# Kernel tuning notes

Measured on AMD Instinct MI355X. Metric: run time of the kernel, lower is better.

## Reference

```python
import jax, jax.numpy as jnp
import numpy as np

N_CONS = 100000
N_VARS = 200000
N_EDGES = 2000000
EMB = 64


def _emb(x, w0, b0, w1, b1):
    # Linear -> ReLU -> Linear -> ReLU
    h = jnp.maximum(x @ w0 + b0, 0.0)
    return jnp.maximum(h @ w1 + b1, 0.0)


def _bgc(left, src, dst, ef, right, lw, lb, ew, rw, fw, fb, ow0, ob0, ow1, ob1):
    # message: final(ReLU)(left_lin(right[dst]) + edge_lin(ef) + right_lin(left[src]))
    pre = right[dst] @ lw + lb + ef @ ew + left[src] @ rw          # [E, EMB]
    msg = jnp.maximum(pre, 0.0) @ fw + fb                          # [E, EMB]
    agg = jax.ops.segment_sum(msg, dst, num_segments=right.shape[0])  # [n_right, EMB]
    h = jnp.concatenate([agg, right], axis=-1)                     # [n_right, 2*EMB]
    return jnp.maximum(h @ ow0 + ob0, 0.0) @ ow1 + ob1


def setup_inputs() -> dict:
    key = jax.random.key(0)
    kit = iter(jax.random.split(key, 64))
    f32 = jnp.float32
    def W(i, o):
        return (jax.random.normal(next(kit), (i, o), f32) / np.float32(np.sqrt(i))).astype(f32)
    def B(o):
        return jnp.zeros((o,), f32)

    d = {}
    d['constraint_features'] = jax.random.normal(next(kit), (N_CONS, 5), f32)
    ei_c = jax.random.randint(next(kit), (N_EDGES,), 0, N_CONS)
    ei_v = jax.random.randint(next(kit), (N_EDGES,), 0, N_VARS)
    d['edge_indices'] = jnp.stack([ei_c, ei_v]).astype(jnp.int32)  # [2, E]
    d['edge_features'] = jax.random.normal(next(kit), (N_EDGES, 1), f32)
    d['variable_features'] = jax.random.normal(next(kit), (N_VARS, 19), f32)

    # cons / var embeddings
    d['cw0'], d['cb0'], d['cw1'], d['cb1'] = W(5, EMB), B(EMB), W(EMB, EMB), B(EMB)
    d['vw0'], d['vb0'], d['vw1'], d['vb1'] = W(19, EMB), B(EMB), W(EMB, EMB), B(EMB)
    # two bipartite convs
    for p in ('vc', 'cv'):
        d[p + '_lw'], d[p + '_lb'] = W(EMB, EMB), B(EMB)
        d[p + '_ew'] = W(1, EMB)
        d[p + '_rw'] = W(EMB, EMB)
        d[p + '_fw'], d[p + '_fb'] = W(EMB, EMB), B(EMB)
        d[p + '_ow0'], d[p + '_ob0'] = W(2 * EMB, EMB), B(EMB)
        d[p + '_ow1'], d[p + '_ob1'] = W(EMB, EMB), B(EMB)
    # policy head (final Linear has no bias)
    d['pw0'], d['pb0'], d['pw1'] = W(EMB, EMB), B(EMB), W(EMB, 1)
    # value head
    d['vhw0'], d['vhb0'], d['vhw1'], d['vhb1'] = W(EMB, EMB), B(EMB), W(EMB, 1), B(1)
    return d


def reference(constraint_features, edge_indices, edge_features, variable_features,
              cw0, cb0, cw1, cb1, vw0, vb0, vw1, vb1,
              vc_lw, vc_lb, vc_ew, vc_rw, vc_fw, vc_fb, vc_ow0, vc_ob0, vc_ow1, vc_ob1,
              cv_lw, cv_lb, cv_ew, cv_rw, cv_fw, cv_fb, cv_ow0, cv_ob0, cv_ow1, cv_ob1,
              pw0, pb0, pw1, vhw0, vhb0, vhw1, vhb1):
    cons_idx = edge_indices[0]
    var_idx = edge_indices[1]
    c = _emb(constraint_features, cw0, cb0, cw1, cb1)  # [n_cons, EMB]
    v = _emb(variable_features, vw0, vb0, vw1, vb1)    # [n_vars, EMB]
    # v -> c (reversed edges: src=var, dst=cons)
    c = _bgc(v, var_idx, cons_idx, edge_features, c,
             vc_lw, vc_lb, vc_ew, vc_rw, vc_fw, vc_fb, vc_ow0, vc_ob0, vc_ow1, vc_ob1)
    # c -> v (src=cons, dst=var)
    v = _bgc(c, cons_idx, var_idx, edge_features, v,
             cv_lw, cv_lb, cv_ew, cv_rw, cv_fw, cv_fb, cv_ow0, cv_ob0, cv_ow1, cv_ob1)
    policy = (jnp.maximum(v @ pw0 + pb0, 0.0) @ pw1).squeeze(-1)   # [n_vars]
    value = (jnp.maximum(v @ vhw0 + vhb0, 0.0) @ vhw1 + vhb1).squeeze(-1)  # [n_vars]
    return (value, policy)
```

## Files before the change

kernel.cpp:

```cpp
#include <hip/hip_runtime.h>

typedef unsigned short u16;

#define RN  128
#define RSH 7
#define CAP 6400
#define NBINS_MAX 4096

__device__ __forceinline__ float bf2f(u16 u) {
    return __uint_as_float(((unsigned int)u) << 16);
}
__device__ __forceinline__ u16 f2bf(float f) {
    unsigned int x = __float_as_uint(f);
    return (u16)((x + 0x7fffu + ((x >> 16) & 1u)) >> 16);
}

__device__ __forceinline__ void mm64(const float* A, const float* B, float* C, int lane)
{
    float bcol[64];
#pragma unroll
    for (int m = 0; m < 64; ++m) bcol[m] = B[m*64 + lane];
    for (int k = 0; k < 64; ++k) {
        float acc = 0.f;
#pragma unroll
        for (int m = 0; m < 64; ++m) acc = fmaf(A[k*64 + m], bcol[m], acc);
        C[k*64 + lane] = acc;
    }
}

__device__ __forceinline__ void vm64(const float* a, const float* B, const float* add,
                                     float* c, int lane)
{
    float acc = (add != 0) ? add[lane] : 0.f;
#pragma unroll
    for (int m = 0; m < 64; ++m) acc = fmaf(a[m], B[m*64 + lane], acc);
    c[lane] = acc;
}

__global__ __launch_bounds__(256) void prep_kernel(
    const float* vc_fw, const float* vc_fb, const float* vc_ow0,
    const float* vc_ow1, const float* vc_ob1,
    const float* cv_rw, const float* cv_fw, const float* cv_fb,
    const float* cv_ow0, const float* cv_ow1, const float* cv_ob1,
    const float* pw0, const float* pb0, const float* vhw0, const float* vhb0,
    float* Fc, float* gc, float* Hc, float* hc, float* Fv, float* gv,
    float* Pw, float* pbp, float* Vw, float* vbp)
{
    const int wv = threadIdx.x >> 6;
    const int lane = threadIdx.x & 63;
    if (wv == 0) {
        mm64(vc_fw, vc_ow0, Fc, lane);
        vm64(vc_fb, vc_ow0, 0, gc, lane);
    } else if (wv == 1) {
        mm64(vc_ow1, cv_rw, Hc, lane);
        vm64(vc_ob1, cv_rw, 0, hc, lane);
    } else if (wv == 2) {
        mm64(cv_fw, cv_ow0, Fv, lane);
        vm64(cv_fb, cv_ow0, 0, gv, lane);
    } else {
        mm64(cv_ow1, pw0, Pw, lane);
        vm64(cv_ob1, pw0, pb0, pbp, lane);
        mm64(cv_ow1, vhw0, Vw, lane);
        vm64(cv_ob1, vhw0, vhb0, vbp, lane);
    }
}

__global__ __launch_bounds__(256) void embc_kernel(
    const float* __restrict__ X,
    const float* __restrict__ W0, const float* __restrict__ B0,
    const float* __restrict__ W1, const float* __restrict__ B1,
    const float* __restrict__ LW, const float* __restrict__ LB,
    u16* __restrict__ c0out, float* __restrict__ RlOut, int M)
{
    const int lane = threadIdx.x & 63;
    const int wv   = threadIdx.x >> 6;
    __shared__ __align__(16) float xs[4][8*5];
    __shared__ __align__(16) float hb[4][8][64];
    __shared__ __align__(16) float yb[4][8][64];
    const int rowTile = (blockIdx.x*4 + wv)*8;

    for (int idx = lane; idx < 8*5; idx += 64) {
        long gi = (long)rowTile*5 + idx;
        xs[wv][idx] = (gi < (long)M*5) ? X[gi] : 0.f;
    }
    {
        float w0[5];
#pragma unroll
        for (int k = 0; k < 5; ++k) w0[k] = W0[k*64 + lane];
        const float b0 = B0[lane];
#pragma unroll
        for (int r = 0; r < 8; ++r) {
            float acc = b0;
#pragma unroll
            for (int k = 0; k < 5; ++k) acc = fmaf(xs[wv][r*5 + k], w0[k], acc);
            hb[wv][r][lane] = fmaxf(acc, 0.f);
        }
    }
    {
        float w1[64];
#pragma unroll
        for (int k = 0; k < 64; ++k) w1[k] = W1[k*64 + lane];
        const float b1 = B1[lane];
#pragma unroll
        for (int r = 0; r < 8; ++r) {
            float acc = b1;
#pragma unroll
            for (int k4 = 0; k4 < 16; ++k4) {
                float4 h4 = *(const float4*)&hb[wv][r][k4*4];
                acc = fmaf(h4.x, w1[k4*4+0], acc);
                acc = fmaf(h4.y, w1[k4*4+1], acc);
                acc = fmaf(h4.z, w1[k4*4+2], acc);
                acc = fmaf(h4.w, w1[k4*4+3], acc);
            }
            float y = fmaxf(acc, 0.f);
            yb[wv][r][lane] = y;
            int row = rowTile + r;
            if (row < M) c0out[(size_t)row*64 + lane] = f2bf(y);
        }
    }
    {
        float w[64];
#pragma unroll
        for (int k = 0; k < 64; ++k) w[k] = LW[k*64 + lane];
        const float bb = LB[lane];
#pragma unroll
        for (int r = 0; r < 8; ++r) {
            float acc = bb;
#pragma unroll
            for (int k4 = 0; k4 < 16; ++k4) {
                float4 y4 = *(const float4*)&yb[wv][r][k4*4];
                acc = fmaf(y4.x, w[k4*4+0], acc);
                acc = fmaf(y4.y, w[k4*4+1], acc);
                acc = fmaf(y4.z, w[k4*4+2], acc);
                acc = fmaf(y4.w, w[k4*4+3], acc);
            }
            int row = rowTile + r;
            if (row < M) RlOut[(size_t)row*64 + lane] = acc;
        }
    }
}

__global__ __launch_bounds__(256) void embv_kernel(
    const float* __restrict__ X,
    const float* __restrict__ W0, const float* __restrict__ B0,
    const float* __restrict__ W1, const float* __restrict__ B1,
    const float* __restrict__ RW,
    const float* __restrict__ LW, const float* __restrict__ LB,
    u16* __restrict__ v0out, u16* __restrict__ LsOut,
    float* __restrict__ RlOut, int M)
{
    const int lane = threadIdx.x & 63;
    const int wv   = threadIdx.x >> 6;
    __shared__ __align__(16) float xs[4][8*19];
    __shared__ __align__(16) float hb[4][8][64];
    __shared__ __align__(16) float yb[4][8][64];
    const int rowTile = (blockIdx.x*4 + wv)*8;

    for (int idx = lane; idx < 8*19; idx += 64) {
        long gi = (long)rowTile*19 + idx;
        xs[wv][idx] = (gi < (long)M*19) ? X[gi] : 0.f;
    }
    {
        float w0[19];
#pragma unroll
        for (int k = 0; k < 19; ++k) w0[k] = W0[k*64 + lane];
        const float b0 = B0[lane];
#pragma unroll
        for (int r = 0; r < 8; ++r) {
            float acc = b0;
#pragma unroll
            for (int k = 0; k < 19; ++k) acc = fmaf(xs[wv][r*19 + k], w0[k], acc);
            hb[wv][r][lane] = fmaxf(acc, 0.f);
        }
    }
    {
        float w1[64];
#pragma unroll
        for (int k = 0; k < 64; ++k) w1[k] = W1[k*64 + lane];
        const float b1 = B1[lane];
#pragma unroll
        for (int r = 0; r < 8; ++r) {
            float acc = b1;
#pragma unroll
            for (int k4 = 0; k4 < 16; ++k4) {
                float4 h4 = *(const float4*)&hb[wv][r][k4*4];
                acc = fmaf(h4.x, w1[k4*4+0], acc);
                acc = fmaf(h4.y, w1[k4*4+1], acc);
                acc = fmaf(h4.z, w1[k4*4+2], acc);
                acc = fmaf(h4.w, w1[k4*4+3], acc);
            }
            float y = fmaxf(acc, 0.f);
            yb[wv][r][lane] = y;
            int row = rowTile + r;
            if (row < M) v0out[(size_t)row*64 + lane] = f2bf(y);
        }
    }
    {
        float w[64];
#pragma unroll
        for (int k = 0; k < 64; ++k) w[k] = RW[k*64 + lane];
#pragma unroll
        for (int r = 0; r < 8; ++r) {
            float acc = 0.f;
#pragma unroll
            for (int k4 = 0; k4 < 16; ++k4) {
                float4 y4 = *(const float4*)&yb[wv][r][k4*4];
                acc = fmaf(y4.x, w[k4*4+0], acc);
                acc = fmaf(y4.y, w[k4*4+1], acc);
                acc = fmaf(y4.z, w[k4*4+2], acc);
                acc = fmaf(y4.w, w[k4*4+3], acc);
            }
            int row = rowTile + r;
            if (row < M) LsOut[(size_t)row*64 + lane] = f2bf(acc);
        }
    }
    {
        float w[64];
#pragma unroll
        for (int k = 0; k < 64; ++k) w[k] = LW[k*64 + lane];
        const float bb = LB[lane];
#pragma unroll
        for (int r = 0; r < 8; ++r) {
            float acc = bb;
#pragma unroll
            for (int k4 = 0; k4 < 16; ++k4) {
                float4 y4 = *(const float4*)&yb[wv][r][k4*4];
                acc = fmaf(y4.x, w[k4*4+0], acc);
                acc = fmaf(y4.y, w[k4*4+1], acc);
                acc = fmaf(y4.z, w[k4*4+2], acc);
                acc = fmaf(y4.w, w[k4*4+3], acc);
            }
            int row = rowTile + r;
            if (row < M) RlOut[(size_t)row*64 + lane] = acc;
        }
    }
}

__global__ __launch_bounds__(256) void hist2_kernel(
    const int* __restrict__ eic, const int* __restrict__ eiv,
    int* cntC, int* cntV, int E)
{
    int e = blockIdx.x*256 + threadIdx.x;
    if (e >= E) return;
    atomicAdd(&cntC[eic[e]], 1);
    atomicAdd(&cntV[eiv[e]], 1);
}

__global__ __launch_bounds__(256) void coarse_kernel(
    const int* __restrict__ cnt, int N, int nb, int* cOff, int* cur)
{
    __shared__ int cs[2049];
    for (int i = threadIdx.x; i < nb; i += 256) {
        int s = 0;
        int basei = i << RSH;
        int lim = N - basei; if (lim > RN) lim = RN;
        for (int j = 0; j < lim; ++j) s += cnt[basei + j];
        cs[i] = s;
    }
    __syncthreads();
    if (threadIdx.x == 0) {
        int a = 0;
        for (int i = 0; i < nb; ++i) { int t = cs[i]; cs[i] = a; a += t; }
        cs[nb] = a;
    }
    __syncthreads();
    for (int i = threadIdx.x; i < nb; i += 256) { cOff[i] = cs[i]; cur[i] = cs[i]; }
    if (threadIdx.x == 0) cOff[nb] = cs[nb];
}

__global__ __launch_bounds__(256) void binscatter_kernel(
    const int* __restrict__ eic, const int* __restrict__ eiv,
    const float* __restrict__ ef,
    int* curC, int* curV,
    uint2* __restrict__ bC, uint2* __restrict__ bV,
    int nbC, int nbV, int E)
{
    __shared__ int bins[NBINS_MAX];
    const int nb = nbC + nbV;
    const int chunk = (E + (int)gridDim.x - 1) / (int)gridDim.x;
    const int e0 = blockIdx.x * chunk;
    int e1 = e0 + chunk; if (e1 > E) e1 = E;

    for (int i = threadIdx.x; i < nb; i += 256) bins[i] = 0;
    __syncthreads();

    for (int e = e0 + threadIdx.x; e < e1; e += 256) {
        atomicAdd(&bins[eic[e] >> RSH], 1);
        atomicAdd(&bins[nbC + (eiv[e] >> RSH)], 1);
    }
    __syncthreads();

    for (int i = threadIdx.x; i < nbC; i += 256) {
        int c = bins[i];
        bins[i] = (c > 0) ? atomicAdd(&curC[i], c) : 0;
    }
    for (int i = threadIdx.x; i < nbV; i += 256) {
        int c = bins[nbC + i];
        bins[nbC + i] = (c > 0) ? atomicAdd(&curV[i], c) : 0;
    }
    __syncthreads();

    for (int e = e0 + threadIdx.x; e < e1; e += 256) {
        const int c = eic[e], v = eiv[e];
        const unsigned fb = __float_as_uint(ef[e]) & 0xFFFFFF80u;
        int pc = atomicAdd(&bins[c >> RSH], 1);
        bC[pc] = make_uint2((unsigned)v, fb | (unsigned)(c & (RN - 1)));
        int pv = atomicAdd(&bins[nbC + (v >> RSH)], 1);
        bV[pv] = make_uint2((unsigned)c, fb | (unsigned)(v & (RN - 1)));
    }
}

__global__ __launch_bounds__(256) void aggsort_kernel(
    const int* __restrict__ cOff, const uint2* __restrict__ bucket,
    float* RlA, const u16* __restrict__ Lsb,
    const float* __restrict__ ew, int N)
{
    const int b = blockIdx.x;
    const int lane = threadIdx.x & 63;
    const int wv   = threadIdx.x >> 6;
    const int n0 = b << RSH;
    int nn = N - n0; if (nn > RN) nn = RN;

    __shared__ uint2 recS[CAP];
    __shared__ int cntS[RN];
    __shared__ int offS[RN + 1];

    const int e0 = cOff[b];
    int ec = cOff[b + 1] - e0;
    if (ec > CAP) ec = CAP;

    for (int i = threadIdx.x; i < RN; i += 256) cntS[i] = 0;
    __syncthreads();
    for (int i = threadIdx.x; i < ec; i += 256) {
        uint2 q = bucket[e0 + i];
        atomicAdd(&cntS[q.y & (RN - 1)], 1);
    }
    __syncthreads();
    if (threadIdx.x == 0) {
        int a = 0;
        for (int i = 0; i < RN; ++i) { offS[i] = a; a += cntS[i]; }
        offS[RN] = a;
    }
    __syncthreads();
    for (int i = threadIdx.x; i < RN; i += 256) cntS[i] = offS[i];
    __syncthreads();
    for (int i = threadIdx.x; i < ec; i += 256) {
        uint2 q = bucket[e0 + i];
        int p = atomicAdd(&cntS[q.y & (RN - 1)], 1);
        recS[p] = q;
    }
    __syncthreads();

    const float w = ew[lane];
    for (int r = wv; r < nn; r += 4) {
        const int s0 = offS[r], s1 = offS[r + 1];
        const float rl = RlA[(size_t)(n0 + r)*64 + lane];
        float acc = 0.f;
        int j = s0;
        for (; j + 8 <= s1; j += 8) {
            uint2 q0 = recS[j+0], q1 = recS[j+1], q2 = recS[j+2], q3 = recS[j+3];
            uint2 q4 = recS[j+4], q5 = recS[j+5], q6 = recS[j+6], q7 = recS[j+7];
            float l0 = bf2f(Lsb[(size_t)q0.x*64 + lane]);
            float l1 = bf2f(Lsb[(size_t)q1.x*64 + lane]);
            float l2 = bf2f(Lsb[(size_t)q2.x*64 + lane]);
            float l3 = bf2f(Lsb[(size_t)q3.x*64 + lane]);
            float l4 = bf2f(Lsb[(size_t)q4.x*64 + lane]);
            float l5 = bf2f(Lsb[(size_t)q5.x*64 + lane]);
            float l6 = bf2f(Lsb[(size_t)q6.x*64 + lane]);
            float l7 = bf2f(Lsb[(size_t)q7.x*64 + lane]);
            float f0 = __uint_as_float(q0.y & 0xFFFFFF80u);
            float f1 = __uint_as_float(q1.y & 0xFFFFFF80u);
            float f2 = __uint_as_float(q2.y & 0xFFFFFF80u);
            float f3 = __uint_as_float(q3.y & 0xFFFFFF80u);
            float f4 = __uint_as_float(q4.y & 0xFFFFFF80u);
            float f5 = __uint_as_float(q5.y & 0xFFFFFF80u);
            float f6 = __uint_as_float(q6.y & 0xFFFFFF80u);
            float f7 = __uint_as_float(q7.y & 0xFFFFFF80u);
            acc += fmaxf(fmaf(f0, w, rl + l0), 0.f);
            acc += fmaxf(fmaf(f1, w, rl + l1), 0.f);
            acc += fmaxf(fmaf(f2, w, rl + l2), 0.f);
            acc += fmaxf(fmaf(f3, w, rl + l3), 0.f);
            acc += fmaxf(fmaf(f4, w, rl + l4), 0.f);
            acc += fmaxf(fmaf(f5, w, rl + l5), 0.f);
            acc += fmaxf(fmaf(f6, w, rl + l6), 0.f);
            acc += fmaxf(fmaf(f7, w, rl + l7), 0.f);
        }
        for (; j < s1; ++j) {
            uint2 q = recS[j];
            float l = bf2f(Lsb[(size_t)q.x*64 + lane]);
            float f = __uint_as_float(q.y & 0xFFFFFF80u);
            acc += fmaxf(fmaf(f, w, rl + l), 0.f);
        }
        RlA[(size_t)(n0 + r)*64 + lane] = acc;
    }
}

__global__ __launch_bounds__(256, 1) void consupd_kernel(
    const float* __restrict__ aggpre, const u16* __restrict__ c0,
    const int* __restrict__ deg,
    const float* __restrict__ Fc, const float* __restrict__ OW0B,
    const float* __restrict__ gc, const float* __restrict__ ob0,
    const float* __restrict__ Hc, const float* __restrict__ hc,
    u16* __restrict__ LsOut, int M)
{
    const int lane = threadIdx.x & 63;
    const int wv   = threadIdx.x >> 6;
    __shared__ __align__(16) float xs[4][8][64];
    __shared__ __align__(16) float cs[4][8][64];
    const int rowTile = (blockIdx.x*4 + wv)*8;

    float degv[8];
#pragma unroll
    for (int r = 0; r < 8; ++r) {
        int row = rowTile + r;
        int grow = (row < M) ? row : (M - 1);
        xs[wv][r][lane] = aggpre[(size_t)grow*64 + lane];
        cs[wv][r][lane] = bf2f(c0[(size_t)grow*64 + lane]);
        degv[r] = (float)deg[grow];
    }
    {
        float wa[64], wb[64];
#pragma unroll
        for (int k = 0; k < 64; ++k) { wa[k] = Fc[k*64 + lane]; wb[k] = OW0B[k*64 + lane]; }
        const float g_l = gc[lane], b_l = ob0[lane];
#pragma unroll
        for (int r = 0; r < 8; ++r) {
            float acc = fmaf(degv[r], g_l, b_l);
#pragma unroll
            for (int k4 = 0; k4 < 16; ++k4) {
                float4 x4 = *(const float4*)&xs[wv][r][k4*4];
                float4 c4 = *(const float4*)&cs[wv][r][k4*4];
                acc = fmaf(x4.x, wa[k4*4+0], acc); acc = fmaf(c4.x, wb[k4*4+0], acc);
                acc = fmaf(x4.y, wa[k4*4+1], acc); acc = fmaf(c4.y, wb[k4*4+1], acc);
                acc = fmaf(x4.z, wa[k4*4+2], acc); acc = fmaf(c4.z, wb[k4*4+2], acc);
                acc = fmaf(x4.w, wa[k4*4+3], acc); acc = fmaf(c4.w, wb[k4*4+3], acc);
            }
            xs[wv][r][lane] = fmaxf(acc, 0.f);
        }
    }
    {
        float wh[64];
#pragma unroll
        for (int k = 0; k < 64; ++k) wh[k] = Hc[k*64 + lane];
        const float h_l = hc[lane];
#pragma unroll
        for (int r = 0; r < 8; ++r) {
            float acc = h_l;
#pragma unroll
            for (int k4 = 0; k4 < 16; ++k4) {
                float4 u4 = *(const float4*)&xs[wv][r][k4*4];
                acc = fmaf(u4.x, wh[k4*4+0], acc);
                acc = fmaf(u4.y, wh[k4*4+1], acc);
                acc = fmaf(u4.z, wh[k4*4+2], acc);
                acc = fmaf(u4.w, wh[k4*4+3], acc);
            }
            int row = rowTile + r;
            if (row < M) LsOut[(size_t)row*64 + lane] = f2bf(acc);
        }
    }
}

__global__ __launch_bounds__(256, 1) void varupdhead_kernel(
    const float* __restrict__ aggpre, const u16* __restrict__ v0,
    const int* __restrict__ deg,
    const float* __restrict__ Fv, const float* __restrict__ OW0B,
    const float* __restrict__ gv, const float* __restrict__ ob0,
    const float* __restrict__ Pw, const float* __restrict__ pbp, const float* __restrict__ pw1,
    const float* __restrict__ Vw, const float* __restrict__ vbp, const float* __restrict__ vw1,
    const float* __restrict__ vb1,
    float* __restrict__ out, int M)
{
    const int lane = threadIdx.x & 63;
    const int wv   = threadIdx.x >> 6;
    __shared__ __align__(16) float xs[4][8][64];
    __shared__ __align__(16) float cs[4][8][64];
    const int rowTile = (blockIdx.x*4 + wv)*8;

    float degv[8];
#pragma unroll
    for (int r = 0; r < 8; ++r) {
        int row = rowTile + r;
        int grow = (row < M) ? row : (M - 1);
        xs[wv][r][lane] = aggpre[(size_t)grow*64 + lane];
        cs[wv][r][lane] = bf2f(v0[(size_t)grow*64 + lane]);
        degv[r] = (float)deg[grow];
    }
    {
        float wa[64], wb[64];
#pragma unroll
        for (int k = 0; k < 64; ++k) { wa[k] = Fv[k*64 + lane]; wb[k] = OW0B[k*64 + lane]; }
        const float g_l = gv[lane], b_l = ob0[lane];
#pragma unroll
        for (int r = 0; r < 8; ++r) {
            float acc = fmaf(degv[r], g_l, b_l);
#pragma unroll
            for (int k4 = 0; k4 < 16; ++k4) {
                float4 x4 = *(const float4*)&xs[wv][r][k4*4];
                float4 c4 = *(const float4*)&cs[wv][r][k4*4];
                acc = fmaf(x4.x, wa[k4*4+0], acc); acc = fmaf(c4.x, wb[k4*4+0], acc);
                acc = fmaf(x4.y, wa[k4*4+1], acc); acc = fmaf(c4.y, wb[k4*4+1], acc);
                acc = fmaf(x4.z, wa[k4*4+2], acc); acc = fmaf(c4.z, wb[k4*4+2], acc);
                acc = fmaf(x4.w, wa[k4*4+3], acc); acc = fmaf(c4.w, wb[k4*4+3], acc);
            }
            xs[wv][r][lane] = fmaxf(acc, 0.f);
        }
    }
    {
        float wp[64], wq[64];
#pragma unroll
        for (int k = 0; k < 64; ++k) { wp[k] = Pw[k*64 + lane]; wq[k] = Vw[k*64 + lane]; }
        const float pb_l = pbp[lane], vb_l = vbp[lane];
        const float p1w = pw1[lane], v1w = vw1[lane];
        const float vbias = vb1[0];
#pragma unroll
        for (int r = 0; r < 8; ++r) {
            float tp = pb_l, tv = vb_l;
#pragma unroll
            for (int k4 = 0; k4 < 16; ++k4) {
                float4 u4 = *(const float4*)&xs[wv][r][k4*4];
                tp = fmaf(u4.x, wp[k4*4+0], tp); tv = fmaf(u4.x, wq[k4*4+0], tv);
                tp = fmaf(u4.y, wp[k4*4+1], tp); tv = fmaf(u4.y, wq[k4*4+1], tv);
                tp = fmaf(u4.z, wp[k4*4+2], tp); tv = fmaf(u4.z, wq[k4*4+2], tv);
                tp = fmaf(u4.w, wp[k4*4+3], tp); tv = fmaf(u4.w, wq[k4*4+3], tv);
            }
            tp = fmaxf(tp, 0.f) * p1w;
            tv = fmaxf(tv, 0.f) * v1w;
#pragma unroll
            for (int m = 32; m >= 1; m >>= 1) {
                tp += __shfl_xor(tp, m, 64);
                tv += __shfl_xor(tv, m, 64);
            }
            int row = rowTile + r;
            if (lane == 0 && row < M) {
                out[row]     = tv + vbias;
                out[M + row] = tp;
            }
        }
    }
}

#define AL256(x) (((x) + 255) & ~(size_t)255)

extern "C" void kernel_launch(void* const* d_in, const int* in_sizes, int n_in,
                              void* d_out, int out_size, void* d_ws, size_t ws_size,
                              hipStream_t stream)
{
    const float* cf  = (const float*)d_in[0];
    const int*   ei  = (const int*)  d_in[1];
    const float* ef  = (const float*)d_in[2];
    const float* vf  = (const float*)d_in[3];

    const float* cw0 = (const float*)d_in[4];
    const float* cb0 = (const float*)d_in[5];
    const float* cw1 = (const float*)d_in[6];
    const float* cb1 = (const float*)d_in[7];
    const float* vw0 = (const float*)d_in[8];
    const float* vb0 = (const float*)d_in[9];
    const float* vw1 = (const float*)d_in[10];
    const float* vb1 = (const float*)d_in[11];

    const float* vc_lw  = (const float*)d_in[12];
    const float* vc_lb  = (const float*)d_in[13];
    const float* vc_ew  = (const float*)d_in[14];
    const float* vc_rw  = (const float*)d_in[15];
    const float* vc_fw  = (const float*)d_in[16];
    const float* vc_fb  = (const float*)d_in[17];
    const float* vc_ow0 = (const float*)d_in[18];
    const float* vc_ob0 = (const float*)d_in[19];
    const float* vc_ow1 = (const float*)d_in[20];
    const float* vc_ob1 = (const float*)d_in[21];

    const float* cv_lw  = (const float*)d_in[22];
    const float* cv_lb  = (const float*)d_in[23];
    const float* cv_ew  = (const float*)d_in[24];
    const float* cv_rw  = (const float*)d_in[25];
    const float* cv_fw  = (const float*)d_in[26];
    const float* cv_fb  = (const float*)d_in[27];
    const float* cv_ow0 = (const float*)d_in[28];
    const float* cv_ob0 = (const float*)d_in[29];
    const float* cv_ow1 = (const float*)d_in[30];
    const float* cv_ob1 = (const float*)d_in[31];

    const float* pw0  = (const float*)d_in[32];
    const float* pb0  = (const float*)d_in[33];
    const float* pw1  = (const float*)d_in[34];
    const float* vhw0 = (const float*)d_in[35];
    const float* vhb0 = (const float*)d_in[36];
    const float* vhw1 = (const float*)d_in[37];
    const float* vhb1 = (const float*)d_in[38];

    const int NC = in_sizes[0] / 5;
    const int E  = in_sizes[1] / 2;
    const int NV = in_sizes[3] / 19;
    const int* eic = ei;
    const int* eiv = ei + E;

    const int nbC = (NC + RN - 1) >> RSH;
    const int nbV = (NV + RN - 1) >> RSH;

    char* base = (char*)d_ws;
    size_t o = 0;
    float*  RlC = (float*)(base + o);  o += AL256((size_t)NC*64*4);
    u16*    c0b = (u16*)  (base + o);  o += AL256((size_t)NC*64*2);
    u16*    LsC = (u16*)  (base + o);  o += AL256((size_t)NC*64*2);
    float*  RlV = (float*)(base + o);  o += AL256((size_t)NV*64*4);
    u16*    v0b = (u16*)  (base + o);  o += AL256((size_t)NV*64*2);
    u16*    LsV = (u16*)  (base + o);  o += AL256((size_t)NV*64*2);
    uint2*  bktC = (uint2*)(base + o); o += AL256((size_t)E*8);
    uint2*  bktV = (uint2*)(base + o); o += AL256((size_t)E*8);
    int* cntC  = (int*)(base + o);  o += AL256((size_t)NC*4);
    int* cntV  = (int*)(base + o);  o += AL256((size_t)NV*4);
    int* cOffC = (int*)(base + o);  o += AL256(((size_t)nbC + 1)*4);
    int* curC  = (int*)(base + o);  o += AL256((size_t)nbC*4);
    int* cOffV = (int*)(base + o);  o += AL256(((size_t)nbV + 1)*4);
    int* curV  = (int*)(base + o);  o += AL256((size_t)nbV*4);
    float* Fc  = (float*)(base + o); o += AL256((size_t)4096*4);
    float* Hc  = (float*)(base + o); o += AL256((size_t)4096*4);
    float* Fv  = (float*)(base + o); o += AL256((size_t)4096*4);
    float* Pw  = (float*)(base + o); o += AL256((size_t)4096*4);
    float* Vw  = (float*)(base + o); o += AL256((size_t)4096*4);
    float* gc  = (float*)(base + o); o += AL256((size_t)64*4);
    float* hc  = (float*)(base + o); o += AL256((size_t)64*4);
    float* gv  = (float*)(base + o); o += AL256((size_t)64*4);
    float* pbp = (float*)(base + o); o += AL256((size_t)64*4);
    float* vbp = (float*)(base + o); o += AL256((size_t)64*4);

    if (o > ws_size) return;
    if (nbC + nbV > NBINS_MAX) return;

    dim3 blk(256);
    dim3 gRowsC((unsigned)((NC + 31) / 32));
    dim3 gRowsV((unsigned)((NV + 31) / 32));
    dim3 gE((unsigned)((E + 255) / 256));

    (void)hipMemsetAsync(cntC, 0, (size_t)NC*4, stream);
    (void)hipMemsetAsync(cntV, 0, (size_t)NV*4, stream);
    hist2_kernel<<<gE, blk, 0, stream>>>(eic, eiv, cntC, cntV, E);
    coarse_kernel<<<dim3(1), blk, 0, stream>>>(cntC, NC, nbC, cOffC, curC);
    coarse_kernel<<<dim3(1), blk, 0, stream>>>(cntV, NV, nbV, cOffV, curV);

    prep_kernel<<<dim3(1), blk, 0, stream>>>(
        vc_fw, vc_fb, vc_ow0, vc_ow1, vc_ob1,
        cv_rw, cv_fw, cv_fb, cv_ow0, cv_ow1, cv_ob1,
        pw0, pb0, vhw0, vhb0,
        Fc, gc, Hc, hc, Fv, gv, Pw, pbp, Vw, vbp);

    embc_kernel<<<gRowsC, blk, 0, stream>>>(cf, cw0, cb0, cw1, cb1,
                                            vc_lw, vc_lb, c0b, RlC, NC);
    embv_kernel<<<gRowsV, blk, 0, stream>>>(vf, vw0, vb0, vw1, vb1,
                                            vc_rw, cv_lw, cv_lb, v0b, LsV, RlV, NV);

    binscatter_kernel<<<dim3(128), blk, 0, stream>>>(eic, eiv, ef, curC, curV,
                                                     bktC, bktV, nbC, nbV, E);

    aggsort_kernel<<<dim3((unsigned)nbC), blk, 0, stream>>>(cOffC, bktC, RlC, LsV, vc_ew, NC);
    consupd_kernel<<<gRowsC, blk, 0, stream>>>(RlC, c0b, cntC,
                                               Fc, vc_ow0 + 64*64, gc, vc_ob0,
                                               Hc, hc, LsC, NC);

    aggsort_kernel<<<dim3((unsigned)nbV), blk, 0, stream>>>(cOffV, bktV, RlV, LsC, cv_ew, NV);
    varupdhead_kernel<<<gRowsV, blk, 0, stream>>>(RlV, v0b, cntV,
                                                  Fv, cv_ow0 + 64*64, gv, cv_ob0,
                                                  Pw, pbp, pw1, Vw, vbp, vhw1, vhb1,
                                                  (float*)d_out, NV);
}
```

Measured before the change: 1.173 ms.

## Split K across waves with LDS atomics in node update kernels to cut registers

The per-node update kernels now give each of the four waves a 16-wide K slice for all 32 rows in the block, instead of having each wave hold full 64-row weight columns. Partial sums are combined with shared-memory atomicAdd, and the launch-bound minimum of one block is dropped. The aim is to shrink per-thread weight registers from 128 to 32 so occupancy rises and the latency of global weight loads is hidden. In exchange it adds LDS atomics, extra barriers and more LDS traffic, and the order of float summation is no longer deterministic.

New measurement: 2.107 ms. 1.8x slower.

```diff
diff --git a/kernel.cpp b/kernel.cpp
--- a/kernel.cpp
+++ b/kernel.cpp
@@ -395,7 +395,7 @@
     }
 }
 
-__global__ __launch_bounds__(256, 1) void consupd_kernel(
+__global__ __launch_bounds__(256) void consupd_kernel(
     const float* __restrict__ aggpre, const u16* __restrict__ c0,
     const int* __restrict__ deg,
     const float* __restrict__ Fc, const float* __restrict__ OW0B,
@@ -405,62 +405,84 @@
 {
     const int lane = threadIdx.x & 63;
     const int wv   = threadIdx.x >> 6;
-    __shared__ __align__(16) float xs[4][8][64];
-    __shared__ __align__(16) float cs[4][8][64];
-    const int rowTile = (blockIdx.x*4 + wv)*8;
-
-    float degv[8];
-#pragma unroll
-    for (int r = 0; r < 8; ++r) {
+    __shared__ __align__(16) float xs[32][64];
+    __shared__ __align__(16) float cs[32][64];
+    __shared__ __align__(16) float accS[32][64];
+    const int rowTile = blockIdx.x * 32;
+    const int k0 = wv * 16;
+
+    const float g_l = gc[lane], b_l = ob0[lane];
+#pragma unroll
+    for (int i = 0; i < 8; ++i) {
+        int r = wv*8 + i;
         int row = rowTile + r;
         int grow = (row < M) ? row : (M - 1);
-        xs[wv][r][lane] = aggpre[(size_t)grow*64 + lane];
-        cs[wv][r][lane] = bf2f(c0[(size_t)grow*64 + lane]);
-        degv[r] = (float)deg[grow];
-    }
-    {
-        float wa[64], wb[64];
-#pragma unroll
-        for (int k = 0; k < 64; ++k) { wa[k] = Fc[k*64 + lane]; wb[k] = OW0B[k*64 + lane]; }
-        const float g_l = gc[lane], b_l = ob0[lane];
-#pragma unroll
-        for (int r = 0; r < 8; ++r) {
-            float acc = fmaf(degv[r], g_l, b_l);
-#pragma unroll
-            for (int k4 = 0; k4 < 16; ++k4) {
-                float4 x4 = *(const float4*)&xs[wv][r][k4*4];
-                float4 c4 = *(const float4*)&cs[wv][r][k4*4];
-                acc = fmaf(x4.x, wa[k4*4+0], acc); acc = fmaf(c4.x, wb[k4*4+0], acc);
-                acc = fmaf(x4.y, wa[k4*4+1], acc); acc = fmaf(c4.y, wb[k4*4+1], acc);
-                acc = fmaf(x4.z, wa[k4*4+2], acc); acc = fmaf(c4.z, wb[k4*4+2], acc);
-                acc = fmaf(x4.w, wa[k4*4+3], acc); acc = fmaf(c4.w, wb[k4*4+3], acc);
-            }
-            xs[wv][r][lane] = fmaxf(acc, 0.f);
-        }
-    }
-    {
-        float wh[64];
-#pragma unroll
-        for (int k = 0; k < 64; ++k) wh[k] = Hc[k*64 + lane];
-        const float h_l = hc[lane];
-#pragma unroll
-        for (int r = 0; r < 8; ++r) {
-            float acc = h_l;
-#pragma unroll
-            for (int k4 = 0; k4 < 16; ++k4) {
-                float4 u4 = *(const float4*)&xs[wv][r][k4*4];
-                acc = fmaf(u4.x, wh[k4*4+0], acc);
-                acc = fmaf(u4.y, wh[k4*4+1], acc);
-                acc = fmaf(u4.z, wh[k4*4+2], acc);
-                acc = fmaf(u4.w, wh[k4*4+3], acc);
-            }
-            int row = rowTile + r;
-            if (row < M) LsOut[(size_t)row*64 + lane] = f2bf(acc);
-        }
-    }
-}
-
-__global__ __launch_bounds__(256, 1) void varupdhead_kernel(
+        xs[r][lane]   = aggpre[(size_t)grow*64 + lane];
+        cs[r][lane]   = bf2f(c0[(size_t)grow*64 + lane]);
+        accS[r][lane] = fmaf((float)deg[grow], g_l, b_l);
+    }
+    __syncthreads();
+
+    {
+        float wa[16], wb[16];
+#pragma unroll
+        for (int j = 0; j < 16; ++j) {
+            wa[j] = Fc[(k0 + j)*64 + lane];
+            wb[j] = OW0B[(k0 + j)*64 + lane];
+        }
+        for (int i = 0; i < 32; ++i) {
+            int r = (wv*8 + i) & 31;
+            float p = 0.f;
+#pragma unroll
+            for (int j4 = 0; j4 < 4; ++j4) {
+                float4 x4 = *(const float4*)&xs[r][k0 + j4*4];
+                float4 c4 = *(const float4*)&cs[r][k0 + j4*4];
+                p = fmaf(x4.x, wa[j4*4+0], p); p = fmaf(c4.x, wb[j4*4+0], p);
+                p = fmaf(x4.y, wa[j4*4+1], p); p = fmaf(c4.y, wb[j4*4+1], p);
+                p = fmaf(x4.z, wa[j4*4+2], p); p = fmaf(c4.z, wb[j4*4+2], p);
+                p = fmaf(x4.w, wa[j4*4+3], p); p = fmaf(c4.w, wb[j4*4+3], p);
+            }
+            atomicAdd(&accS[r][lane], p);
+        }
+    }
+    __syncthreads();
+
+    const float h_l = hc[lane];
+#pragma unroll
+    for (int i = 0; i < 8; ++i) xs[wv*8 + i][lane] = h_l;
+    __syncthreads();
+
+    {
+        float wh[16];
+#pragma unroll
+        for (int j = 0; j < 16; ++j) wh[j] = Hc[(k0 + j)*64 + lane];
+        for (int i = 0; i < 32; ++i) {
+            int r = (wv*8 + i) & 31;
+            float p = 0.f;
+#pragma unroll
+            for (int j4 = 0; j4 < 4; ++j4) {
+                float4 u4 = *(const float4*)&accS[r][k0 + j4*4];
+                u4.x = fmaxf(u4.x, 0.f); u4.y = fmaxf(u4.y, 0.f);
+                u4.z = fmaxf(u4.z, 0.f); u4.w = fmaxf(u4.w, 0.f);
+                p = fmaf(u4.x, wh[j4*4+0], p);
+                p = fmaf(u4.y, wh[j4*4+1], p);
+                p = fmaf(u4.z, wh[j4*4+2], p);
+                p = fmaf(u4.w, wh[j4*4+3], p);
+            }
+            atomicAdd(&xs[r][lane], p);
+        }
+    }
+    __syncthreads();
+
+#pragma unroll
+    for (int i = 0; i < 8; ++i) {
+        int r = wv*8 + i;
+        int row = rowTile + r;
+        if (row < M) LsOut[(size_t)row*64 + lane] = f2bf(xs[r][lane]);
+    }
+}
+
+__global__ __launch_bounds__(256) void varupdhead_kernel(
     const float* __restrict__ aggpre, const u16* __restrict__ v0,
     const int* __restrict__ deg,
     const float* __restrict__ Fv, const float* __restrict__ OW0B,
@@ -472,69 +494,95 @@
 {
     const int lane = threadIdx.x & 63;
     const int wv   = threadIdx.x >> 6;
-    __shared__ __align__(16) float xs[4][8][64];
-    __shared__ __align__(16) float cs[4][8][64];
-    const int rowTile = (blockIdx.x*4 + wv)*8;
-
-    float degv[8];
-#pragma unroll
-    for (int r = 0; r < 8; ++r) {
+    __shared__ __align__(16) float xs[32][64];
+    __shared__ __align__(16) float cs[32][64];
+    __shared__ __align__(16) float accS[32][64];
+    __shared__ __align__(16) float tpS[32][64];
+    __shared__ __align__(16) float tvS[32][64];
+    const int rowTile = blockIdx.x * 32;
+    const int k0 = wv * 16;
+
+    const float g_l = gv[lane], b_l = ob0[lane];
+    const float pb_l = pbp[lane], vb_l = vbp[lane];
+#pragma unroll
+    for (int i = 0; i < 8; ++i) {
+        int r = wv*8 + i;
         int row = rowTile + r;
         int grow = (row < M) ? row : (M - 1);
-        xs[wv][r][lane] = aggpre[(size_t)grow*64 + lane];
-        cs[wv][r][lane] = bf2f(v0[(size_t)grow*64 + lane]);
-        degv[r] = (float)deg[grow];
-    }
-    {
-        float wa[64], wb[64];
-#pragma unroll
-        for (int k = 0; k < 64; ++k) { wa[k] = Fv[k*64 + lane]; wb[k] = OW0B[k*64 + lane]; }
-        const float g_l = gv[lane], b_l = ob0[lane];
-#pragma unroll
-        for (int r = 0; r < 8; ++r) {
-            float acc = fmaf(degv[r], g_l, b_l);
-#pragma unroll
-            for (int k4 = 0; k4 < 16; ++k4) {
-                float4 x4 = *(const float4*)&xs[wv][r][k4*4];
-                float4 c4 = *(const float4*)&cs[wv][r][k4*4];
-                acc = fmaf(x4.x, wa[k4*4+0], acc); acc = fmaf(c4.x, wb[k4*4+0], acc);
-                acc = fmaf(x4.y, wa[k4*4+1], acc); acc = fmaf(c4.y, wb[k4*4+1], acc);
-                acc = fmaf(x4.z, wa[k4*4+2], acc); acc = fmaf(c4.z, wb[k4*4+2], acc);
-                acc = fmaf(x4.w, wa[k4*4+3], acc); acc = fmaf(c4.w, wb[k4*4+3], acc);
-            }
-            xs[wv][r][lane] = fmaxf(acc, 0.f);
-        }
-    }
-    {
-        float wp[64], wq[64];
-#pragma unroll
-        for (int k = 0; k < 64; ++k) { wp[k] = Pw[k*64 + lane]; wq[k] = Vw[k*64 + lane]; }
-        const float pb_l = pbp[lane], vb_l = vbp[lane];
-        const float p1w = pw1[lane], v1w = vw1[lane];
-        const float vbias = vb1[0];
-#pragma unroll
-        for (int r = 0; r < 8; ++r) {
-            float tp = pb_l, tv = vb_l;
-#pragma unroll
-            for (int k4 = 0; k4 < 16; ++k4) {
-                float4 u4 = *(const float4*)&xs[wv][r][k4*4];
-                tp = fmaf(u4.x, wp[k4*4+0], tp); tv = fmaf(u4.x, wq[k4*4+0], tv);
-                tp = fmaf(u4.y, wp[k4*4+1], tp); tv = fmaf(u4.y, wq[k4*4+1], tv);
-                tp = fmaf(u4.z, wp[k4*4+2], tp); tv = fmaf(u4.z, wq[k4*4+2], tv);
-                tp = fmaf(u4.w, wp[k4*4+3], tp); tv = fmaf(u4.w, wq[k4*4+3], tv);
-            }
-            tp = fmaxf(tp, 0.f) * p1w;
-            tv = fmaxf(tv, 0.f) * v1w;
-#pragma unroll
-            for (int m = 32; m >= 1; m >>= 1) {
-                tp += __shfl_xor(tp, m, 64);
-                tv += __shfl_xor(tv, m, 64);
-            }
-            int row = rowTile + r;
-            if (lane == 0 && row < M) {
-                out[row]     = tv + vbias;
-                out[M + row] = tp;
-            }
+        xs[r][lane]   = aggpre[(size_t)grow*64 + lane];
+        cs[r][lane]   = bf2f(v0[(size_t)grow*64 + lane]);
+        accS[r][lane] = fmaf((float)deg[grow], g_l, b_l);
+        tpS[r][lane]  = pb_l;
+        tvS[r][lane]  = vb_l;
+    }
+    __syncthreads();
+
+    {
+        float wa[16], wb[16];
+#pragma unroll
+        for (int j = 0; j < 16; ++j) {
+            wa[j] = Fv[(k0 + j)*64 + lane];
+            wb[j] = OW0B[(k0 + j)*64 + lane];
+        }
+        for (int i = 0; i < 32; ++i) {
+            int r = (wv*8 + i) & 31;
+            float p = 0.f;
+#pragma unroll
+            for (int j4 = 0; j4 < 4; ++j4) {
+                float4 x4 = *(const float4*)&xs[r][k0 + j4*4];
+                float4 c4 = *(const float4*)&cs[r][k0 + j4*4];
+                p = fmaf(x4.x, wa[j4*4+0], p); p = fmaf(c4.x, wb[j4*4+0], p);
+                p = fmaf(x4.y, wa[j4*4+1], p); p = fmaf(c4.y, wb[j4*4+1], p);
+                p = fmaf(x4.z, wa[j4*4+2], p); p = fmaf(c4.z, wb[j4*4+2], p);
+                p = fmaf(x4.w, wa[j4*4+3], p); p = fmaf(c4.w, wb[j4*4+3], p);
+            }
+            atomicAdd(&accS[r][lane], p);
+        }
+    }
+    __syncthreads();
+
+    {
+        float wp[16], wq[16];
+#pragma unroll
+        for (int j = 0; j < 16; ++j) {
+            wp[j] = Pw[(k0 + j)*64 + lane];
+            wq[j] = Vw[(k0 + j)*64 + lane];
+        }
+        for (int i = 0; i < 32; ++i) {
+            int r = (wv*8 + i) & 31;
+            float tp = 0.f, tv = 0.f;
+#pragma unroll
+            for (int j4 = 0; j4 < 4; ++j4) {
+                float4 u4 = *(const float4*)&accS[r][k0 + j4*4];
+                u4.x = fmaxf(u4.x, 0.f); u4.y = fmaxf(u4.y, 0.f);
+                u4.z = fmaxf(u4.z, 0.f); u4.w = fmaxf(u4.w, 0.f);
+                tp = fmaf(u4.x, wp[j4*4+0], tp); tv = fmaf(u4.x, wq[j4*4+0], tv);
+                tp = fmaf(u4.y, wp[j4*4+1], tp); tv = fmaf(u4.y, wq[j4*4+1], tv);
+                tp = fmaf(u4.z, wp[j4*4+2], tp); tv = fmaf(u4.z, wq[j4*4+2], tv);
+                tp = fmaf(u4.w, wp[j4*4+3], tp); tv = fmaf(u4.w, wq[j4*4+3], tv);
+            }
+            atomicAdd(&tpS[r][lane], tp);
+            atomicAdd(&tvS[r][lane], tv);
+        }
+    }
+    __syncthreads();
+
+    const float p1w = pw1[lane], v1w = vw1[lane];
+    const float vbias = vb1[0];
+#pragma unroll
+    for (int i = 0; i < 8; ++i) {
+        int r = wv*8 + i;
+        float a = fmaxf(tpS[r][lane], 0.f) * p1w;
+        float b = fmaxf(tvS[r][lane], 0.f) * v1w;
+#pragma unroll
+        for (int m = 32; m >= 1; m >>= 1) {
+            a += __shfl_xor(a, m, 64);
+            b += __shfl_xor(b, m, 64);
+        }
+        int row = rowTile + r;
+        if (lane == 0 && row < M) {
+            out[row]     = b + vbias;
+            out[M + row] = a;
         }
     }
 }
```

## Split update-kernel matmuls across waves to halve per-wave weight registers

Applied to the files above, without the earlier changes.

The constraint-update and variable-update/head kernels now process a shared 32-row tile per block. Each wave holds only one 64-wide weight column set (Fc/Fv or OW0B, and Pw or Vw in the head) instead of two, and partial sums are combined through shared memory with extra barriers. The launch_bounds min-blocks hint of 1 is dropped so the lower register use can give higher occupancy. This adds shared memory traffic and syncthreads, and the per-wave inner loops are no longer fully unrolled over rows.

Measured after the change: 1.172 ms. No clear change (-0.2%).

```diff
diff --git a/kernel.cpp b/kernel.cpp
--- a/kernel.cpp
+++ b/kernel.cpp
@@ -395,7 +395,7 @@
     }
 }
 
-__global__ __launch_bounds__(256, 1) void consupd_kernel(
+__global__ __launch_bounds__(256) void consupd_kernel(
     const float* __restrict__ aggpre, const u16* __restrict__ c0,
     const int* __restrict__ deg,
     const float* __restrict__ Fc, const float* __restrict__ OW0B,
@@ -405,54 +405,72 @@
 {
     const int lane = threadIdx.x & 63;
     const int wv   = threadIdx.x >> 6;
-    __shared__ __align__(16) float xs[4][8][64];
-    __shared__ __align__(16) float cs[4][8][64];
-    const int rowTile = (blockIdx.x*4 + wv)*8;
-
-    float degv[8];
-#pragma unroll
-    for (int r = 0; r < 8; ++r) {
+    __shared__ __align__(16) float xs[32][64];
+    __shared__ __align__(16) float cs[32][64];
+    __shared__ __align__(16) float pA[32][64];
+    __shared__ __align__(16) float pB[32][64];
+    const int rowTile = blockIdx.x * 32;
+
+    const float g_l = gc[lane], b_l = ob0[lane];
+#pragma unroll
+    for (int i = 0; i < 8; ++i) {
+        int r = wv*8 + i;
         int row = rowTile + r;
         int grow = (row < M) ? row : (M - 1);
-        xs[wv][r][lane] = aggpre[(size_t)grow*64 + lane];
-        cs[wv][r][lane] = bf2f(c0[(size_t)grow*64 + lane]);
-        degv[r] = (float)deg[grow];
-    }
-    {
-        float wa[64], wb[64];
-#pragma unroll
-        for (int k = 0; k < 64; ++k) { wa[k] = Fc[k*64 + lane]; wb[k] = OW0B[k*64 + lane]; }
-        const float g_l = gc[lane], b_l = ob0[lane];
-#pragma unroll
-        for (int r = 0; r < 8; ++r) {
-            float acc = fmaf(degv[r], g_l, b_l);
-#pragma unroll
-            for (int k4 = 0; k4 < 16; ++k4) {
-                float4 x4 = *(const float4*)&xs[wv][r][k4*4];
-                float4 c4 = *(const float4*)&cs[wv][r][k4*4];
-                acc = fmaf(x4.x, wa[k4*4+0], acc); acc = fmaf(c4.x, wb[k4*4+0], acc);
-                acc = fmaf(x4.y, wa[k4*4+1], acc); acc = fmaf(c4.y, wb[k4*4+1], acc);
-                acc = fmaf(x4.z, wa[k4*4+2], acc); acc = fmaf(c4.z, wb[k4*4+2], acc);
-                acc = fmaf(x4.w, wa[k4*4+3], acc); acc = fmaf(c4.w, wb[k4*4+3], acc);
-            }
-            xs[wv][r][lane] = fmaxf(acc, 0.f);
-        }
-    }
-    {
-        float wh[64];
-#pragma unroll
-        for (int k = 0; k < 64; ++k) wh[k] = Hc[k*64 + lane];
+        xs[r][lane] = aggpre[(size_t)grow*64 + lane];
+        cs[r][lane] = bf2f(c0[(size_t)grow*64 + lane]);
+        pA[r][lane] = fmaf((float)deg[grow], g_l, b_l);
+    }
+    __syncthreads();
+
+    {
+        const bool isB = (wv >= 2);
+        const float* W = isB ? OW0B : Fc;
+        float w[64];
+#pragma unroll
+        for (int k = 0; k < 64; ++k) w[k] = W[k*64 + lane];
+        const int r0 = (wv & 1) * 16;
+        for (int i = 0; i < 16; ++i) {
+            int r = r0 + i;
+            float p = 0.f;
+#pragma unroll
+            for (int k4 = 0; k4 < 16; ++k4) {
+                float4 s4 = isB ? *(const float4*)&cs[r][k4*4]
+                                : *(const float4*)&xs[r][k4*4];
+                p = fmaf(s4.x, w[k4*4+0], p);
+                p = fmaf(s4.y, w[k4*4+1], p);
+                p = fmaf(s4.z, w[k4*4+2], p);
+                p = fmaf(s4.w, w[k4*4+3], p);
+            }
+            if (isB) pB[r][lane] = p;
+            else     pA[r][lane] += p;
+        }
+    }
+    __syncthreads();
+
+#pragma unroll
+    for (int i = 0; i < 8; ++i) {
+        int r = wv*8 + i;
+        xs[r][lane] = fmaxf(pA[r][lane] + pB[r][lane], 0.f);
+    }
+    __syncthreads();
+
+    {
+        float w[64];
+#pragma unroll
+        for (int k = 0; k < 64; ++k) w[k] = Hc[k*64 + lane];
         const float h_l = hc[lane];
 #pragma unroll
-        for (int r = 0; r < 8; ++r) {
+        for (int i = 0; i < 8; ++i) {
+            int r = wv*8 + i;
             float acc = h_l;
 #pragma unroll
             for (int k4 = 0; k4 < 16; ++k4) {
-                float4 u4 = *(const float4*)&xs[wv][r][k4*4];
-                acc = fmaf(u4.x, wh[k4*4+0], acc);
-                acc = fmaf(u4.y, wh[k4*4+1], acc);
-                acc = fmaf(u4.z, wh[k4*4+2], acc);
-                acc = fmaf(u4.w, wh[k4*4+3], acc);
+                float4 u4 = *(const float4*)&xs[r][k4*4];
+                acc = fmaf(u4.x, w[k4*4+0], acc);
+                acc = fmaf(u4.y, w[k4*4+1], acc);
+                acc = fmaf(u4.z, w[k4*4+2], acc);
+                acc = fmaf(u4.w, w[k4*4+3], acc);
             }
             int row = rowTile + r;
             if (row < M) LsOut[(size_t)row*64 + lane] = f2bf(acc);
@@ -460,7 +478,7 @@
     }
 }
 
-__global__ __launch_bounds__(256, 1) void varupdhead_kernel(
+__global__ __launch_bounds__(256) void varupdhead_kernel(
     const float* __restrict__ aggpre, const u16* __restrict__ v0,
     const int* __restrict__ deg,
     const float* __restrict__ Fv, const float* __restrict__ OW0B,
@@ -472,68 +490,84 @@
 {
     const int lane = threadIdx.x & 63;
     const int wv   = threadIdx.x >> 6;
-    __shared__ __align__(16) float xs[4][8][64];
-    __shared__ __align__(16) float cs[4][8][64];
-    const int rowTile = (blockIdx.x*4 + wv)*8;
-
-    float degv[8];
-#pragma unroll
-    for (int r = 0; r < 8; ++r) {
+    __shared__ __align__(16) float xs[32][64];
+    __shared__ __align__(16) float cs[32][64];
+    __shared__ __align__(16) float pA[32][64];
+    __shared__ __align__(16) float pB[32][64];
+    const int rowTile = blockIdx.x * 32;
+
+    const float g_l = gv[lane], b_l = ob0[lane];
+#pragma unroll
+    for (int i = 0; i < 8; ++i) {
+        int r = wv*8 + i;
         int row = rowTile + r;
         int grow = (row < M) ? row : (M - 1);
-        xs[wv][r][lane] = aggpre[(size_t)grow*64 + lane];
-        cs[wv][r][lane] = bf2f(v0[(size_t)grow*64 + lane]);
-        degv[r] = (float)deg[grow];
-    }
-    {
-        float wa[64], wb[64];
-#pragma unroll
-        for (int k = 0; k < 64; ++k) { wa[k] = Fv[k*64 + lane]; wb[k] = OW0B[k*64 + lane]; }
-        const float g_l = gv[lane], b_l = ob0[lane];
-#pragma unroll
-        for (int r = 0; r < 8; ++r) {
-            float acc = fmaf(degv[r], g_l, b_l);
-#pragma unroll
-            for (int k4 = 0; k4 < 16; ++k4) {
-                float4 x4 = *(const float4*)&xs[wv][r][k4*4];
-                float4 c4 = *(const float4*)&cs[wv][r][k4*4];
-                acc = fmaf(x4.x, wa[k4*4+0], acc); acc = fmaf(c4.x, wb[k4*4+0], acc);
-                acc = fmaf(x4.y, wa[k4*4+1], acc); acc = fmaf(c4.y, wb[k4*4+1], acc);
-                acc = fmaf(x4.z, wa[k4*4+2], acc); acc = fmaf(c4.z, wb[k4*4+2], acc);
-                acc = fmaf(x4.w, wa[k4*4+3], acc); acc = fmaf(c4.w, wb[k4*4+3], acc);
-            }
-            xs[wv][r][lane] = fmaxf(acc, 0.f);
-        }
-    }
-    {
-        float wp[64], wq[64];
-#pragma unroll
-        for (int k = 0; k < 64; ++k) { wp[k] = Pw[k*64 + lane]; wq[k] = Vw[k*64 + lane]; }
-        const float pb_l = pbp[lane], vb_l = vbp[lane];
-        const float p1w = pw1[lane], v1w = vw1[lane];
-        const float vbias = vb1[0];
-#pragma unroll
-        for (int r = 0; r < 8; ++r) {
-            float tp = pb_l, tv = vb_l;
-#pragma unroll
-            for (int k4 = 0; k4 < 16; ++k4) {
-                float4 u4 = *(const float4*)&xs[wv][r][k4*4];
-                tp = fmaf(u4.x, wp[k4*4+0], tp); tv = fmaf(u4.x, wq[k4*4+0], tv);
-                tp = fmaf(u4.y, wp[k4*4+1], tp); tv = fmaf(u4.y, wq[k4*4+1], tv);
-                tp = fmaf(u4.z, wp[k4*4+2], tp); tv = fmaf(u4.z, wq[k4*4+2], tv);
-                tp = fmaf(u4.w, wp[k4*4+3], tp); tv = fmaf(u4.w, wq[k4*4+3], tv);
-            }
-            tp = fmaxf(tp, 0.f) * p1w;
-            tv = fmaxf(tv, 0.f) * v1w;
-#pragma unroll
-            for (int m = 32; m >= 1; m >>= 1) {
-                tp += __shfl_xor(tp, m, 64);
-                tv += __shfl_xor(tv, m, 64);
-            }
+        xs[r][lane] = aggpre[(size_t)grow*64 + lane];
+        cs[r][lane] = bf2f(v0[(size_t)grow*64 + lane]);
+        pA[r][lane] = fmaf((float)deg[grow], g_l, b_l);
+    }
+    __syncthreads();
+
+    {
+        const bool isB = (wv >= 2);
+        const float* W = isB ? OW0B : Fv;
+        float w[64];
+#pragma unroll
+        for (int k = 0; k < 64; ++k) w[k] = W[k*64 + lane];
+        const int r0 = (wv & 1) * 16;
+        for (int i = 0; i < 16; ++i) {
+            int r = r0 + i;
+            float p = 0.f;
+#pragma unroll
+            for (int k4 = 0; k4 < 16; ++k4) {
+                float4 s4 = isB ? *(const float4*)&cs[r][k4*4]
+                                : *(const float4*)&xs[r][k4*4];
+                p = fmaf(s4.x, w[k4*4+0], p);
+                p = fmaf(s4.y, w[k4*4+1], p);
+                p = fmaf(s4.z, w[k4*4+2], p);
+                p = fmaf(s4.w, w[k4*4+3], p);
+            }
+            if (isB) pB[r][lane] = p;
+            else     pA[r][lane] += p;
+        }
+    }
+    __syncthreads();
+
+#pragma unroll
+    for (int i = 0; i < 8; ++i) {
+        int r = wv*8 + i;
+        xs[r][lane] = fmaxf(pA[r][lane] + pB[r][lane], 0.f);
+    }
+    __syncthreads();
+
+    {
+        const bool isV = (wv >= 2);
+        const float* W = isV ? Vw : Pw;
+        const float bias_l = isV ? vbp[lane] : pbp[lane];
+        const float mul_l  = isV ? vw1[lane] : pw1[lane];
+        const float vbias  = vb1[0];
+        float w[64];
+#pragma unroll
+        for (int k = 0; k < 64; ++k) w[k] = W[k*64 + lane];
+        const int r0 = (wv & 1) * 16;
+        for (int i = 0; i < 16; ++i) {
+            int r = r0 + i;
+            float t = bias_l;
+#pragma unroll
+            for (int k4 = 0; k4 < 16; ++k4) {
+                float4 u4 = *(const float4*)&xs[r][k4*4];
+                t = fmaf(u4.x, w[k4*4+0], t);
+                t = fmaf(u4.y, w[k4*4+1], t);
+                t = fmaf(u4.z, w[k4*4+2], t);
+                t = fmaf(u4.w, w[k4*4+3], t);
+            }
+            t = fmaxf(t, 0.f) * mul_l;
+#pragma unroll
+            for (int m = 32; m >= 1; m >>= 1) t += __shfl_xor(t, m, 64);
             int row = rowTile + r;
             if (lane == 0 && row < M) {
-                out[row]     = tv + vbias;
-                out[M + row] = tp;
+                if (isV) out[row]     = t + vbias;
+                else     out[M + row] = t;
             }
         }
     }
```
